# Optimization experiments

Measured on AMD Instinct MI355X. Metric: run time of the kernel, lower is better.

The kernel has to match this reference:

```python
import jax, jax.numpy as jnp
import numpy as np

D_MODEL = 1024
NUM_HEADS = 16
WINDOW = 2048  # must equal seq_len (see notes): source matmul attn(B,H,S,W) @ v(B,H,S,hd) requires W == S
SEQ_LEN = 2048
BATCH = 1


def setup_inputs() -> dict:
    key = jax.random.key(0)
    k0, k1, k2 = jax.random.split(key, 3)
    d = D_MODEL
    x = jax.random.normal(k0, (BATCH, SEQ_LEN, d), dtype=jnp.float32)
    w_qkv = jax.random.normal(k1, (3 * d, d), dtype=jnp.float32) * (d ** -0.5)
    b_qkv = jnp.zeros((3 * d,), dtype=jnp.float32)
    w_proj = jax.random.normal(k2, (d, d), dtype=jnp.float32) * (d ** -0.5)
    b_proj = jnp.zeros((d,), dtype=jnp.float32)
    return {"x": x, "w_qkv": w_qkv, "b_qkv": b_qkv, "w_proj": w_proj, "b_proj": b_proj}


def reference(x, w_qkv, b_qkv, w_proj, b_proj):
    B, S, d = x.shape
    H = NUM_HEADS
    hd = d // H
    W = WINDOW
    scale = hd ** -0.5

    # qkv projection (torch Linear: x @ W^T + b)
    qkv = x @ w_qkv.T + b_qkv                      # (B, S, 3d)
    qkv = qkv.reshape(B, S, 3, H, hd).transpose(2, 0, 3, 1, 4)  # (3, B, H, S, hd)
    q, k, v = qkv[0], qkv[1], qkv[2]

    # sliding-window scores: score[b,h,i,j] = q_i . k_padded[i+j] * scale, j in [0, W)
    pad = W // 2
    k_pad = jnp.pad(k, ((0, 0), (0, 0), (pad, pad), (0, 0)))     # (B, H, S+W, hd)
    scores_full = jnp.einsum('bhid,bhjd->bhij', q, k_pad) * scale  # (B, H, S, S+W)
    idx = jnp.arange(S)[:, None] + jnp.arange(W)[None, :]          # (S, W) banded gather indices
    scores = jnp.take_along_axis(scores_full, idx[None, None], axis=-1)  # (B, H, S, W)

    attn = jax.nn.softmax(scores, axis=-1)
    attn = jnp.nan_to_num(attn)  # faithful to torch.nan_to_num(attn, 0.0)

    # Faithful to the source: forward() does matmul(attn, v), i.e. column j of the
    # windowed attn indexes v position j directly (requires W == S).
    out = jnp.einsum('bhij,bhjd->bhid', attn, v)   # (B, H, S, hd)
    out = out.transpose(0, 2, 1, 3).reshape(B, S, d)
    out = out @ w_proj.T + b_proj
    return out, attn
```

## Files before the change

### kernel.cpp

```cpp
#include <hip/hip_runtime.h>
#include <hip/hip_bf16.h>

typedef __hip_bfloat16 bf16;
typedef __attribute__((ext_vector_type(8))) short short8;
typedef __attribute__((ext_vector_type(4))) float f32x4;

#define DEV static __device__ __forceinline__

static constexpr int SEQ = 2048;
static constexpr int DM  = 1024;
static constexpr int NH  = 16;
static constexpr int HD  = 64;
static constexpr int WIN = 2048;
static constexpr int PAD = 1024;

DEV void async16(const void* g, void* l) {
  __builtin_amdgcn_global_load_lds(
      (__attribute__((address_space(1))) void*)(g),
      (__attribute__((address_space(3))) void*)(l), 16, 0, 0);
}

__global__ __launch_bounds__(256) void k_cvt(const float* __restrict__ x,
                                             const float* __restrict__ wq,
                                             const float* __restrict__ wp,
                                             bf16* __restrict__ xb,
                                             bf16* __restrict__ wqb,
                                             bf16* __restrict__ wpb) {
  const int NX = SEQ * DM, NQ = 3 * DM * DM, NP = DM * DM;
  const int tot = (NX + NQ + NP) >> 2;
  const int stride = gridDim.x * 256;
  for (int i = blockIdx.x * 256 + threadIdx.x; i < tot; i += stride) {
    int e = i << 2;
    const float* s; bf16* d; int o;
    if (e < NX)            { s = x;  d = xb;  o = e; }
    else if (e < NX + NQ)  { s = wq; d = wqb; o = e - NX; }
    else                   { s = wp; d = wpb; o = e - NX - NQ; }
    float4 v = *(const float4*)(s + o);
    __align__(8) bf16 t4[4] = {__float2bfloat16(v.x), __float2bfloat16(v.y),
                               __float2bfloat16(v.z), __float2bfloat16(v.w)};
    *(uint2*)(d + o) = *(uint2*)t4;
  }
}

DEV void gemm_core(const bf16* __restrict__ A, const bf16* __restrict__ B,
                   int m0, int n0, int K, int tid, bf16* As, bf16* Bs,
                   f32x4 (&acc)[4][4]) {
  const int lane = tid & 63, wid = tid >> 6;
  const int wm = wid >> 1, wn = wid & 1;
  const int l15 = lane & 15, l4 = lane >> 4;
  for (int k0 = 0; k0 < K; k0 += 64) {
    __syncthreads();
    #pragma unroll
    for (int it = 0; it < 4; ++it) {
      int rb = it * 32 + wid * 8;
      int r  = rb + (lane >> 3);
      int c  = (lane & 7) * 8;
      async16(A + (size_t)(m0 + r) * K + k0 + c, As + rb * 64);
      async16(B + (size_t)(n0 + r) * K + k0 + c, Bs + rb * 64);
    }
    asm volatile("s_waitcnt vmcnt(0)" ::: "memory");
    __syncthreads();
    #pragma unroll
    for (int kk = 0; kk < 2; ++kk) {
      short8 a[4], b[4];
      #pragma unroll
      for (int im = 0; im < 4; ++im)
        a[im] = *(const short8*)(As + (wm * 64 + im * 16 + l15) * 64 + kk * 32 + l4 * 8);
      #pragma unroll
      for (int in = 0; in < 4; ++in)
        b[in] = *(const short8*)(Bs + (wn * 64 + in * 16 + l15) * 64 + kk * 32 + l4 * 8);
      #pragma unroll
      for (int im = 0; im < 4; ++im)
        #pragma unroll
        for (int in = 0; in < 4; ++in)
          acc[im][in] = __builtin_amdgcn_mfma_f32_16x16x32_bf16(a[im], b[in], acc[im][in], 0, 0, 0);
    }
  }
}

__global__ __launch_bounds__(256) void k_gemm_qkv(const bf16* __restrict__ A,
                                                  const bf16* __restrict__ B,
                                                  const float* __restrict__ bias,
                                                  bf16* __restrict__ qo,
                                                  bf16* __restrict__ ko,
                                                  bf16* __restrict__ vt) {
  __shared__ bf16 As[128 * 64], Bs[128 * 64];
  const int tid = threadIdx.x, lane = tid & 63;
  const int wid = tid >> 6, wm = wid >> 1, wn = wid & 1;
  const int l15 = lane & 15, l4 = lane >> 4;
  const int m0 = blockIdx.x * 128, n0 = blockIdx.y * 128;
  f32x4 acc[4][4] = {};
  gemm_core(A, B, m0, n0, DM, tid, As, Bs, acc);
  #pragma unroll
  for (int im = 0; im < 4; ++im)
    #pragma unroll
    for (int in = 0; in < 4; ++in) {
      int col = n0 + wn * 64 + in * 16 + l15;
      float bval = bias[col];
      int t = col >> 10, h = (col >> 6) & 15, dd = col & 63;
      int row0 = m0 + wm * 64 + im * 16 + l4 * 4;
      if (t == 2) {
        __align__(8) bf16 t4[4];
        #pragma unroll
        for (int r = 0; r < 4; ++r)
          t4[r] = __float2bfloat16(acc[im][in][r] + bval);
        *(uint2*)&vt[((size_t)h * HD + dd) * SEQ + row0] = *(uint2*)t4;
      } else {
        #pragma unroll
        for (int r = 0; r < 4; ++r) {
          float v = acc[im][in][r] + bval;
          size_t idx = ((size_t)h * SEQ + row0 + r) * HD + dd;
          if (t == 0) qo[idx] = __float2bfloat16(v * 0.18033688011112042f);
          else        ko[idx] = __float2bfloat16(v);
        }
      }
    }
}

DEV void stage_kp(const bf16* kbase, int i0, int tt, int lane, bf16* dst) {
  #pragma unroll
  for (int it = 0; it < 4; ++it) {
    int r  = it * 8 + (lane >> 3);
    int cg = lane & 7;
    int jp = i0 + tt * 32 + r;
    int krow = jp - PAD;
    krow = krow < 0 ? 0 : (krow > SEQ - 1 ? SEQ - 1 : krow);
    int sc = (cg ^ (r & 7)) * 8;
    async16(kbase + (size_t)krow * HD + sc, dst + it * 8 * 64);
  }
}

DEV void load_kf(const bf16* kbase, int i0, int tt, int l15, int l4,
                 short8 (&kf)[2][2]) {
  #pragma unroll
  for (int fn = 0; fn < 2; ++fn) {
    int jp = i0 + tt * 32 + fn * 16 + l15;
    int krow = jp - PAD;
    krow = krow < 0 ? 0 : (krow > SEQ - 1 ? SEQ - 1 : krow);
    const bf16* rp = kbase + (size_t)krow * HD + l4 * 8;
    kf[fn][0] = *(const short8*)(rp);
    kf[fn][1] = *(const short8*)(rp + 32);
  }
}

DEV void qk_mfma_sw(const short8 (&kf)[2][2], const short8 (&qf)[2][2],
                    f32x4 (&sf)[2][2]) {
  __builtin_amdgcn_s_setprio(1);
  #pragma unroll
  for (int kg = 0; kg < 2; ++kg)
    #pragma unroll
    for (int fj = 0; fj < 2; ++fj)
      #pragma unroll
      for (int fi = 0; fi < 2; ++fi)
        sf[fj][fi] = __builtin_amdgcn_mfma_f32_16x16x32_bf16(kf[fj][kg], qf[fi][kg], sf[fj][fi], 0, 0, 0);
  __builtin_amdgcn_s_setprio(0);
}

DEV int pad_lo(int i0) { int d = PAD - i0; return d <= 0 ? 0 : (d >> 5); }
DEV int pad_hi(int i0) { int t = ((PAD + SEQ - 1 - i0) >> 5) + 1; return t > 65 ? 65 : t; }

__global__ __launch_bounds__(64) void k_attn1(const bf16* __restrict__ q,
                                              const bf16* __restrict__ kkk,
                                              float* __restrict__ psums,
                                              float* __restrict__ aof) {
  const int c  = blockIdx.x & 3;
  const int i0 = ((blockIdx.x >> 2) & 63) << 5;
  const int h  = blockIdx.x >> 8;
  const int lane = threadIdx.x;
  const int l15 = lane & 15, l4 = lane >> 4;

  {
    f32x4 z = {0.f, 0.f, 0.f, 0.f};
    ((f32x4*)aof)[blockIdx.x * 128 + lane]      = z;
    ((f32x4*)aof)[blockIdx.x * 128 + 64 + lane] = z;
  }

  constexpr int st[5] = {0, 16, 32, 48, 65};
  const int lo_g = pad_lo(i0), hi_g = pad_hi(i0);
  int lo = st[c] > lo_g ? st[c] : lo_g;
  int hi = st[c + 1] < hi_g ? st[c + 1] : hi_g;

  short8 qf[2][2];
  #pragma unroll
  for (int fi = 0; fi < 2; ++fi)
    #pragma unroll
    for (int kg = 0; kg < 2; ++kg)
      qf[fi][kg] = *(const short8*)&q[((size_t)h * SEQ + i0 + fi * 16 + l15) * HD + kg * 32 + l4 * 8];

  const bf16* kbase = kkk + (size_t)h * SEQ * HD;

  float psum[2] = {0.f, 0.f};
  auto acc_tile = [&](const f32x4 (&sf)[2][2], int tt) {
    const bool interior = (tt >= 1) && (tt <= 63) &&
                          (i0 + tt * 32 >= PAD) && (i0 + tt * 32 + 31 < PAD + SEQ);
    if (interior) {
      #pragma unroll
      for (int fj = 0; fj < 2; ++fj)
        #pragma unroll
        for (int r = 0; r < 4; ++r) {
          psum[0] += __builtin_amdgcn_exp2f(sf[fj][0][r]);
          psum[1] += __builtin_amdgcn_exp2f(sf[fj][1][r]);
        }
    } else {
      #pragma unroll
      for (int fj = 0; fj < 2; ++fj)
        #pragma unroll
        for (int r = 0; r < 4; ++r) {
          int jj = tt * 32 + fj * 16 + l4 * 4 + r;
          int jp = i0 + jj;
          bool pad = (jp < PAD) || (jp >= PAD + SEQ);
          #pragma unroll
          for (int fi = 0; fi < 2; ++fi) {
            int iloc = fi * 16 + l15;
            float e = pad ? 1.0f : __builtin_amdgcn_exp2f(sf[fj][fi][r]);
            if ((unsigned)(jj - iloc) < (unsigned)WIN) psum[fi] += e;
          }
        }
    }
  };

  short8 kA[2][2], kB[2][2];
  if (lo < hi) load_kf(kbase, i0, lo, l15, l4, kA);
  for (int tt = lo; tt < hi; ++tt) {
    if (((tt - lo) & 1) == 0) {
      if (tt + 1 < hi) load_kf(kbase, i0, tt + 1, l15, l4, kB);
      f32x4 sf[2][2] = {};
      qk_mfma_sw(kA, qf, sf);
      acc_tile(sf, tt);
    } else {
      if (tt + 1 < hi) load_kf(kbase, i0, tt + 1, l15, l4, kA);
      f32x4 sf[2][2] = {};
      qk_mfma_sw(kB, qf, sf);
      acc_tile(sf, tt);
    }
  }

  float r0 = psum[0];
  r0 += __shfl_xor(r0, 16); r0 += __shfl_xor(r0, 32);
  float r1 = psum[1];
  r1 += __shfl_xor(r1, 16); r1 += __shfl_xor(r1, 32);
  if (lane < 32) {
    int i_abs = i0 + lane;
    float s = (lane < 16) ? r0 : r1;
    if (c == 0) {
      int cl = i0 + lo_g * 32 - i_abs; if (cl < 0) cl = 0;
      int cr = i_abs + WIN - (i0 + hi_g * 32); if (cr < 0) cr = 0;
      s += (float)(cl + cr);
    }
    psums[((size_t)c * NH + h) * SEQ + i_abs] = s;
  }
}

__global__ __launch_bounds__(64) void k_attn2(const bf16* __restrict__ q,
                                              const bf16* __restrict__ kkk,
                                              const bf16* __restrict__ vT,
                                              const float* __restrict__ psums,
                                              float* __restrict__ attn,
                                              float* __restrict__ aof) {
  const int c  = blockIdx.x & 3;
  const int i0 = ((blockIdx.x >> 2) & 63) << 5;
  const int h  = blockIdx.x >> 8;
  const int lane = threadIdx.x;
  const int l15 = lane & 15, l4 = lane >> 4;
  const int c0 = c * 16, c1 = c0 + 16;
  const int lo_g = pad_lo(i0), hi_g = pad_hi(i0);

  __shared__ bf16 KP[2][32 * 64];
  __shared__ float JF[32 * 64];

  float inv[2][4];
  #pragma unroll
  for (int fm = 0; fm < 2; ++fm)
    #pragma unroll
    for (int r = 0; r < 4; ++r) {
      int row = i0 + fm * 16 + l4 * 4 + r;
      float s = 0.f;
      #pragma unroll
      for (int cc = 0; cc < 4; ++cc)
        s += psums[((size_t)cc * NH + h) * SEQ + row];
      inv[fm][r] = __builtin_amdgcn_rcpf(s);
    }

  short8 qf[2][2];
  #pragma unroll
  for (int fm = 0; fm < 2; ++fm)
    #pragma unroll
    for (int kg = 0; kg < 2; ++kg)
      qf[fm][kg] = *(const short8*)&q[((size_t)h * SEQ + i0 + fm * 16 + l15) * HD + kg * 32 + l4 * 8];

  const bf16* kbase = kkk + (size_t)h * SEQ * HD;
  const bf16* vbase = vT + (size_t)h * HD * SEQ;
  float* abase = attn + (size_t)(h * SEQ + i0) * WIN;

  f32x4 oacc[2][4] = {};
  stage_kp(kbase, i0, c0, lane, KP[0]);
  for (int tt = c0; tt <= c1; ++tt) {
    short8 bv[4];
    if (tt > c0) {
      int jb = (tt - 1) * 32;
      #pragma unroll
      for (int nd = 0; nd < 4; ++nd)
        bv[nd] = *(const short8*)&vbase[(size_t)(nd * 16 + l15) * SEQ + jb + l4 * 8];
    }
    int nxt = (tt < c1) ? tt + 1 : tt;
    stage_kp(kbase, i0, nxt, lane, KP[(tt + 1) & 1]);
    if (tt == c0)          asm volatile("s_waitcnt vmcnt(4)" ::: "memory");
    else if (tt == c0 + 1) asm volatile("s_waitcnt vmcnt(8)" ::: "memory");
    else                   asm volatile("s_waitcnt vmcnt(12)" ::: "memory");

    const bool fp = (tt < lo_g) || (tt >= hi_g);
    f32x4 sf[2][2] = {};
    if (!fp) {
      const bf16* KPb = KP[tt & 1];
      __builtin_amdgcn_s_setprio(1);
      #pragma unroll
      for (int kg = 0; kg < 2; ++kg) {
        short8 kfr[2];
        #pragma unroll
        for (int fn = 0; fn < 2; ++fn) {
          int jl = fn * 16 + l15;
          int pg = (kg * 4 + l4) ^ (jl & 7);
          kfr[fn] = *(const short8*)&KPb[jl * 64 + pg * 8];
        }
        #pragma unroll
        for (int fm = 0; fm < 2; ++fm)
          #pragma unroll
          for (int fn = 0; fn < 2; ++fn)
            sf[fm][fn] = __builtin_amdgcn_mfma_f32_16x16x32_bf16(qf[fm][kg], kfr[fn], sf[fm][fn], 0, 0, 0);
      }
      __builtin_amdgcn_s_setprio(0);
    }

    const bool allv = (i0 + tt * 32 >= PAD) && (i0 + tt * 32 + 31 < PAD + SEQ);
    #pragma unroll
    for (int fm = 0; fm < 2; ++fm)
      #pragma unroll
      for (int fn = 0; fn < 2; ++fn) {
        int J0 = tt * 32 + fn * 16 + l15;
        bool padc = fp || (!allv && ((i0 + J0 < PAD) || (i0 + J0 >= PAD + SEQ)));
        #pragma unroll
        for (int r = 0; r < 4; ++r) {
          int row = fm * 16 + l4 * 4 + r;
          float e = padc ? 1.0f : __builtin_amdgcn_exp2f(sf[fm][fn][r]);
          float val = e * inv[fm][r];
          int j6 = (J0 - row) & 63;
          int pgrp = (j6 >> 2) ^ ((row & 7) << 1);
          JF[row * 64 + pgrp * 4 + (j6 & 3)] = val;
        }
      }

    if (tt > c0) {
      const int g = (tt - 1) & 1;
      const int Jb = (tt - 1) * 32;
      #pragma unroll
      for (int s = 0; s < 4; ++s) {
        int row = s * 8 + (lane >> 3);
        int c8 = lane & 7;
        int pgrp = (g * 8 + c8) ^ ((row & 7) << 1);
        f32x4 vv = *(const f32x4*)&JF[row * 64 + pgrp * 4];
        __builtin_nontemporal_store(vv, (f32x4*)(abase + (size_t)row * WIN + Jb + c8 * 4));
      }
      short8 af[2];
      #pragma unroll
      for (int fm = 0; fm < 2; ++fm) {
        int row = fm * 16 + l15;
        int pg0 = (g * 8 + l4 * 2) ^ ((row & 7) << 1);
        const float* p = &JF[row * 64 + pg0 * 4];
        union { unsigned short u[8]; short8 v; } tmp;
        #pragma unroll
        for (int e = 0; e < 8; ++e)
          tmp.u[e] = __bfloat16_as_ushort(__float2bfloat16(p[e]));
        af[fm] = tmp.v;
      }
      __builtin_amdgcn_s_setprio(1);
      #pragma unroll
      for (int fm = 0; fm < 2; ++fm)
        #pragma unroll
        for (int nd = 0; nd < 4; ++nd)
          oacc[fm][nd] = __builtin_amdgcn_mfma_f32_16x16x32_bf16(af[fm], bv[nd], oacc[fm][nd], 0, 0, 0);
      __builtin_amdgcn_s_setprio(0);
    }
  }
  #pragma unroll
  for (int fm = 0; fm < 2; ++fm)
    #pragma unroll
    for (int nd = 0; nd < 4; ++nd)
      #pragma unroll
      for (int r = 0; r < 4; ++r) {
        int i  = i0 + fm * 16 + l4 * 4 + r;
        int dd = nd * 16 + l15;
        atomicAdd(&aof[((size_t)h * SEQ + i) * HD + dd], oacc[fm][nd][r]);
      }
}

__global__ __launch_bounds__(256) void k_ored(const float* __restrict__ aof,
                                              bf16* __restrict__ ao) {
  int f = blockIdx.x * 256 + threadIdx.x;
  int e = f << 2;
  int h  = e >> 17;
  int i  = (e >> 6) & (SEQ - 1);
  int dd = e & 63;
  float4 v = ((const float4*)aof)[f];
  __align__(8) bf16 t4[4] = {__float2bfloat16(v.x), __float2bfloat16(v.y),
                             __float2bfloat16(v.z), __float2bfloat16(v.w)};
  *(uint2*)&ao[(size_t)i * DM + h * HD + dd] = *(uint2*)t4;
}

__global__ __launch_bounds__(256) void k_gemm_proj(const bf16* __restrict__ A,
                                                   const bf16* __restrict__ B,
                                                   const float* __restrict__ bias,
                                                   float* __restrict__ out) {
  __shared__ bf16 As[128 * 64], Bs[128 * 64];
  const int tid = threadIdx.x, lane = tid & 63;
  const int wid = tid >> 6, wm = wid >> 1, wn = wid & 1;
  const int l15 = lane & 15, l4 = lane >> 4;
  const int m0 = blockIdx.x * 128, n0 = blockIdx.y * 128;
  f32x4 acc[4][4] = {};
  gemm_core(A, B, m0, n0, DM, tid, As, Bs, acc);
  #pragma unroll
  for (int im = 0; im < 4; ++im)
    #pragma unroll
    for (int in = 0; in < 4; ++in) {
      int col = n0 + wn * 64 + in * 16 + l15;
      float bval = bias[col];
      #pragma unroll
      for (int r = 0; r < 4; ++r) {
        int row = m0 + wm * 64 + im * 16 + l4 * 4 + r;
        out[(size_t)row * DM + col] = acc[im][in][r] + bval;
      }
    }
}

extern "C" void kernel_launch(void* const* d_in, const int* in_sizes, int n_in,
                              void* d_out, int out_size, void* d_ws, size_t ws_size,
                              hipStream_t stream) {
  (void)in_sizes; (void)n_in; (void)out_size; (void)ws_size;
  const float* x  = (const float*)d_in[0];
  const float* wq = (const float*)d_in[1];
  const float* bq = (const float*)d_in[2];
  const float* wp = (const float*)d_in[3];
  const float* bp = (const float*)d_in[4];
  float* out  = (float*)d_out;
  float* attn = out + (size_t)SEQ * DM;

  char* ws = (char*)d_ws;
  bf16* xb    = (bf16*)(ws + (size_t) 0);
  bf16* wqb   = (bf16*)(ws + ((size_t)4  << 20));
  bf16* wpb   = (bf16*)(ws + ((size_t)10 << 20));
  bf16* qarr  = (bf16*)(ws + ((size_t)12 << 20));
  bf16* karr  = (bf16*)(ws + ((size_t)16 << 20));
  bf16* vt    = (bf16*)(ws + ((size_t)24 << 20));
  bf16* ao    = (bf16*)(ws + ((size_t)28 << 20));
  float* aof  = (float*)(ws + (size_t)0);
  float* psums= (float*)(ws + ((size_t)8 << 20));

  k_cvt<<<dim3(1024), dim3(256), 0, stream>>>(x, wq, wp, xb, wqb, wpb);
  k_gemm_qkv<<<dim3(16, 24), dim3(256), 0, stream>>>(xb, wqb, bq, qarr, karr, vt);
  k_attn1<<<dim3(4096), dim3(64), 0, stream>>>(qarr, karr, psums, aof);
  k_attn2<<<dim3(4096), dim3(64), 0, stream>>>(qarr, karr, vt, psums, attn, aof);
  k_ored<<<dim3(NH * SEQ * HD / 4 / 256), dim3(256), 0, stream>>>(aof, ao);
  k_gemm_proj<<<dim3(16, 8), dim3(256), 0, stream>>>(ao, wpb, bp, out);
}
```

Before: 176.8 us.

## Merge four chunk waves per attention block and stage K through LDS in pass one

Both attention kernels now launch 256-thread blocks in which each of four waves handles one column chunk of the same 32-row query tile, replacing four separate 64-thread blocks. Each wave gets its own LDS slices for K and JF. The first pass no longer loads K fragments directly from global into registers; it double-buffers K tiles into swizzled LDS with async global-to-LDS loads and a vmcnt wait, like the second pass already does. The goal is fewer, larger workgroups and cheaper K loads, at the cost of more LDS per block, which may limit occupancy.

```diff
diff --git a/kernel.cpp b/kernel.cpp
--- a/kernel.cpp
+++ b/kernel.cpp
@@ -130,49 +130,69 @@
   }
 }
 
-DEV void load_kf(const bf16* kbase, int i0, int tt, int l15, int l4,
-                 short8 (&kf)[2][2]) {
-  #pragma unroll
-  for (int fn = 0; fn < 2; ++fn) {
-    int jp = i0 + tt * 32 + fn * 16 + l15;
-    int krow = jp - PAD;
-    krow = krow < 0 ? 0 : (krow > SEQ - 1 ? SEQ - 1 : krow);
-    const bf16* rp = kbase + (size_t)krow * HD + l4 * 8;
-    kf[fn][0] = *(const short8*)(rp);
-    kf[fn][1] = *(const short8*)(rp + 32);
-  }
-}
-
-DEV void qk_mfma_sw(const short8 (&kf)[2][2], const short8 (&qf)[2][2],
-                    f32x4 (&sf)[2][2]) {
+DEV void qk_mfma_lds(const bf16* KPb, const short8 (&qf)[2][2], int l15, int l4,
+                     f32x4 (&sf)[2][2]) {
   __builtin_amdgcn_s_setprio(1);
   #pragma unroll
-  for (int kg = 0; kg < 2; ++kg)
+  for (int kg = 0; kg < 2; ++kg) {
+    short8 kfr[2];
+    #pragma unroll
+    for (int fn = 0; fn < 2; ++fn) {
+      int jl = fn * 16 + l15;
+      int pg = (kg * 4 + l4) ^ (jl & 7);
+      kfr[fn] = *(const short8*)&KPb[jl * 64 + pg * 8];
+    }
+    #pragma unroll
+    for (int fm = 0; fm < 2; ++fm)
+      #pragma unroll
+      for (int fn = 0; fn < 2; ++fn)
+        sf[fm][fn] = __builtin_amdgcn_mfma_f32_16x16x32_bf16(qf[fm][kg], kfr[fn], sf[fm][fn], 0, 0, 0);
+  }
+  __builtin_amdgcn_s_setprio(0);
+}
+
+DEV void qk_mfma_lds_sw(const bf16* KPb, const short8 (&qf)[2][2], int l15, int l4,
+                        f32x4 (&sf)[2][2]) {
+  __builtin_amdgcn_s_setprio(1);
+  #pragma unroll
+  for (int kg = 0; kg < 2; ++kg) {
+    short8 kfr[2];
+    #pragma unroll
+    for (int fj = 0; fj < 2; ++fj) {
+      int jl = fj * 16 + l15;
+      int pg = (kg * 4 + l4) ^ (jl & 7);
+      kfr[fj] = *(const short8*)&KPb[jl * 64 + pg * 8];
+    }
     #pragma unroll
     for (int fj = 0; fj < 2; ++fj)
       #pragma unroll
       for (int fi = 0; fi < 2; ++fi)
-        sf[fj][fi] = __builtin_amdgcn_mfma_f32_16x16x32_bf16(kf[fj][kg], qf[fi][kg], sf[fj][fi], 0, 0, 0);
+        sf[fj][fi] = __builtin_amdgcn_mfma_f32_16x16x32_bf16(kfr[fj], qf[fi][kg], sf[fj][fi], 0, 0, 0);
+  }
   __builtin_amdgcn_s_setprio(0);
 }
 
 DEV int pad_lo(int i0) { int d = PAD - i0; return d <= 0 ? 0 : (d >> 5); }
 DEV int pad_hi(int i0) { int t = ((PAD + SEQ - 1 - i0) >> 5) + 1; return t > 65 ? 65 : t; }
 
-__global__ __launch_bounds__(64) void k_attn1(const bf16* __restrict__ q,
-                                              const bf16* __restrict__ kkk,
-                                              float* __restrict__ psums,
-                                              float* __restrict__ aof) {
-  const int c  = blockIdx.x & 3;
-  const int i0 = ((blockIdx.x >> 2) & 63) << 5;
-  const int h  = blockIdx.x >> 8;
-  const int lane = threadIdx.x;
+__global__ __launch_bounds__(256) void k_attn1(const bf16* __restrict__ q,
+                                               const bf16* __restrict__ kkk,
+                                               float* __restrict__ psums,
+                                               float* __restrict__ aof) {
+  const int h  = blockIdx.x >> 6;
+  const int i0 = (blockIdx.x & 63) << 5;
+  const int tid = threadIdx.x;
+  const int c = tid >> 6;
+  const int lane = tid & 63;
   const int l15 = lane & 15, l4 = lane >> 4;
+
+  __shared__ bf16 KP[4][2][32 * 64];
 
   {
     f32x4 z = {0.f, 0.f, 0.f, 0.f};
-    ((f32x4*)aof)[blockIdx.x * 128 + lane]      = z;
-    ((f32x4*)aof)[blockIdx.x * 128 + 64 + lane] = z;
+    size_t zb = ((size_t)h * SEQ + i0) * (HD / 4);
+    ((f32x4*)aof)[zb + tid]       = z;
+    ((f32x4*)aof)[zb + 256 + tid] = z;
   }
 
   constexpr int st[5] = {0, 16, 32, 48, 65};
@@ -190,51 +210,42 @@
   const bf16* kbase = kkk + (size_t)h * SEQ * HD;
 
   float psum[2] = {0.f, 0.f};
-  auto acc_tile = [&](const f32x4 (&sf)[2][2], int tt) {
-    const bool interior = (tt >= 1) && (tt <= 63) &&
-                          (i0 + tt * 32 >= PAD) && (i0 + tt * 32 + 31 < PAD + SEQ);
-    if (interior) {
-      #pragma unroll
-      for (int fj = 0; fj < 2; ++fj)
-        #pragma unroll
-        for (int r = 0; r < 4; ++r) {
-          psum[0] += __builtin_amdgcn_exp2f(sf[fj][0][r]);
-          psum[1] += __builtin_amdgcn_exp2f(sf[fj][1][r]);
-        }
-    } else {
-      #pragma unroll
-      for (int fj = 0; fj < 2; ++fj)
-        #pragma unroll
-        for (int r = 0; r < 4; ++r) {
-          int jj = tt * 32 + fj * 16 + l4 * 4 + r;
-          int jp = i0 + jj;
-          bool pad = (jp < PAD) || (jp >= PAD + SEQ);
+  if (lo < hi) {
+    stage_kp(kbase, i0, lo, lane, KP[c][lo & 1]);
+    for (int tt = lo; tt < hi; ++tt) {
+      int nxt = (tt + 1 < hi) ? tt + 1 : tt;
+      stage_kp(kbase, i0, nxt, lane, KP[c][(tt + 1) & 1]);
+      asm volatile("s_waitcnt vmcnt(4)" ::: "memory");
+      f32x4 sf[2][2] = {};
+      qk_mfma_lds_sw(KP[c][tt & 1], qf, l15, l4, sf);
+      const bool interior = (tt >= 1) && (tt <= 63) &&
+                            (i0 + tt * 32 >= PAD) && (i0 + tt * 32 + 31 < PAD + SEQ);
+      if (interior) {
+        #pragma unroll
+        for (int fj = 0; fj < 2; ++fj)
           #pragma unroll
-          for (int fi = 0; fi < 2; ++fi) {
-            int iloc = fi * 16 + l15;
-            float e = pad ? 1.0f : __builtin_amdgcn_exp2f(sf[fj][fi][r]);
-            if ((unsigned)(jj - iloc) < (unsigned)WIN) psum[fi] += e;
+          for (int r = 0; r < 4; ++r) {
+            psum[0] += __builtin_amdgcn_exp2f(sf[fj][0][r]);
+            psum[1] += __builtin_amdgcn_exp2f(sf[fj][1][r]);
           }
-        }
-    }
-  };
-
-  short8 kA[2][2], kB[2][2];
-  if (lo < hi) load_kf(kbase, i0, lo, l15, l4, kA);
-  for (int tt = lo; tt < hi; ++tt) {
-    if (((tt - lo) & 1) == 0) {
-      if (tt + 1 < hi) load_kf(kbase, i0, tt + 1, l15, l4, kB);
-      f32x4 sf[2][2] = {};
-      qk_mfma_sw(kA, qf, sf);
-      acc_tile(sf, tt);
-    } else {
-      if (tt + 1 < hi) load_kf(kbase, i0, tt + 1, l15, l4, kA);
-      f32x4 sf[2][2] = {};
-      qk_mfma_sw(kB, qf, sf);
-      acc_tile(sf, tt);
-    }
-  }
-
+      } else {
+        #pragma unroll
+        for (int fj = 0; fj < 2; ++fj)
+          #pragma unroll
+          for (int r = 0; r < 4; ++r) {
+            int jj = tt * 32 + fj * 16 + l4 * 4 + r;
+            int jp = i0 + jj;
+            bool pad = (jp < PAD) || (jp >= PAD + SEQ);
+            #pragma unroll
+            for (int fi = 0; fi < 2; ++fi) {
+              int iloc = fi * 16 + l15;
+              float e = pad ? 1.0f : __builtin_amdgcn_exp2f(sf[fj][fi][r]);
+              if ((unsigned)(jj - iloc) < (unsigned)WIN) psum[fi] += e;
+            }
+          }
+      }
+    }
+  }
   float r0 = psum[0];
   r0 += __shfl_xor(r0, 16); r0 += __shfl_xor(r0, 32);
   float r1 = psum[1];
@@ -251,22 +262,23 @@
   }
 }
 
-__global__ __launch_bounds__(64) void k_attn2(const bf16* __restrict__ q,
-                                              const bf16* __restrict__ kkk,
-                                              const bf16* __restrict__ vT,
-                                              const float* __restrict__ psums,
-                                              float* __restrict__ attn,
-                                              float* __restrict__ aof) {
-  const int c  = blockIdx.x & 3;
-  const int i0 = ((blockIdx.x >> 2) & 63) << 5;
-  const int h  = blockIdx.x >> 8;
-  const int lane = threadIdx.x;
+__global__ __launch_bounds__(256) void k_attn2(const bf16* __restrict__ q,
+                                               const bf16* __restrict__ kkk,
+                                               const bf16* __restrict__ vT,
+                                               const float* __restrict__ psums,
+                                               float* __restrict__ attn,
+                                               float* __restrict__ aof) {
+  const int h  = blockIdx.x >> 6;
+  const int i0 = (blockIdx.x & 63) << 5;
+  const int tid = threadIdx.x;
+  const int c = tid >> 6;
+  const int lane = tid & 63;
   const int l15 = lane & 15, l4 = lane >> 4;
   const int c0 = c * 16, c1 = c0 + 16;
   const int lo_g = pad_lo(i0), hi_g = pad_hi(i0);
 
-  __shared__ bf16 KP[2][32 * 64];
-  __shared__ float JF[32 * 64];
+  __shared__ bf16 KP[4][2][32 * 64];
+  __shared__ float JF[4][32 * 64];
 
   float inv[2][4];
   #pragma unroll
@@ -291,9 +303,10 @@
   const bf16* kbase = kkk + (size_t)h * SEQ * HD;
   const bf16* vbase = vT + (size_t)h * HD * SEQ;
   float* abase = attn + (size_t)(h * SEQ + i0) * WIN;
+  float* JFW = JF[c];
 
   f32x4 oacc[2][4] = {};
-  stage_kp(kbase, i0, c0, lane, KP[0]);
+  stage_kp(kbase, i0, c0, lane, KP[c][0]);
   for (int tt = c0; tt <= c1; ++tt) {
     short8 bv[4];
     if (tt > c0) {
@@ -303,33 +316,14 @@
         bv[nd] = *(const short8*)&vbase[(size_t)(nd * 16 + l15) * SEQ + jb + l4 * 8];
     }
     int nxt = (tt < c1) ? tt + 1 : tt;
-    stage_kp(kbase, i0, nxt, lane, KP[(tt + 1) & 1]);
+    stage_kp(kbase, i0, nxt, lane, KP[c][(tt + 1) & 1]);
     if (tt == c0)          asm volatile("s_waitcnt vmcnt(4)" ::: "memory");
     else if (tt == c0 + 1) asm volatile("s_waitcnt vmcnt(8)" ::: "memory");
     else                   asm volatile("s_waitcnt vmcnt(12)" ::: "memory");
 
     const bool fp = (tt < lo_g) || (tt >= hi_g);
     f32x4 sf[2][2] = {};
-    if (!fp) {
-      const bf16* KPb = KP[tt & 1];
-      __builtin_amdgcn_s_setprio(1);
-      #pragma unroll
-      for (int kg = 0; kg < 2; ++kg) {
-        short8 kfr[2];
-        #pragma unroll
-        for (int fn = 0; fn < 2; ++fn) {
-          int jl = fn * 16 + l15;
-          int pg = (kg * 4 + l4) ^ (jl & 7);
-          kfr[fn] = *(const short8*)&KPb[jl * 64 + pg * 8];
-        }
-        #pragma unroll
-        for (int fm = 0; fm < 2; ++fm)
-          #pragma unroll
-          for (int fn = 0; fn < 2; ++fn)
-            sf[fm][fn] = __builtin_amdgcn_mfma_f32_16x16x32_bf16(qf[fm][kg], kfr[fn], sf[fm][fn], 0, 0, 0);
-      }
-      __builtin_amdgcn_s_setprio(0);
-    }
+    if (!fp) qk_mfma_lds(KP[c][tt & 1], qf, l15, l4, sf);
 
     const bool allv = (i0 + tt * 32 >= PAD) && (i0 + tt * 32 + 31 < PAD + SEQ);
     #pragma unroll
@@ -345,7 +339,7 @@
           float val = e * inv[fm][r];
           int j6 = (J0 - row) & 63;
           int pgrp = (j6 >> 2) ^ ((row & 7) << 1);
-          JF[row * 64 + pgrp * 4 + (j6 & 3)] = val;
+          JFW[row * 64 + pgrp * 4 + (j6 & 3)] = val;
         }
       }
 
@@ -357,7 +351,7 @@
         int row = s * 8 + (lane >> 3);
         int c8 = lane & 7;
         int pgrp = (g * 8 + c8) ^ ((row & 7) << 1);
-        f32x4 vv = *(const f32x4*)&JF[row * 64 + pgrp * 4];
+        f32x4 vv = *(const f32x4*)&JFW[row * 64 + pgrp * 4];
         __builtin_nontemporal_store(vv, (f32x4*)(abase + (size_t)row * WIN + Jb + c8 * 4));
       }
       short8 af[2];
@@ -365,7 +359,7 @@
       for (int fm = 0; fm < 2; ++fm) {
         int row = fm * 16 + l15;
         int pg0 = (g * 8 + l4 * 2) ^ ((row & 7) << 1);
-        const float* p = &JF[row * 64 + pg0 * 4];
+        const float* p = &JFW[row * 64 + pg0 * 4];
         union { unsigned short u[8]; short8 v; } tmp;
         #pragma unroll
         for (int e = 0; e < 8; ++e)
@@ -456,8 +450,8 @@
 
   k_cvt<<<dim3(1024), dim3(256), 0, stream>>>(x, wq, wp, xb, wqb, wpb);
   k_gemm_qkv<<<dim3(16, 24), dim3(256), 0, stream>>>(xb, wqb, bq, qarr, karr, vt);
-  k_attn1<<<dim3(4096), dim3(64), 0, stream>>>(qarr, karr, psums, aof);
-  k_attn2<<<dim3(4096), dim3(64), 0, stream>>>(qarr, karr, vt, psums, attn, aof);
+  k_attn1<<<dim3(1024), dim3(256), 0, stream>>>(qarr, karr, psums, aof);
+  k_attn2<<<dim3(1024), dim3(256), 0, stream>>>(qarr, karr, vt, psums, attn, aof);
   k_ored<<<dim3(NH * SEQ * HD / 4 / 256), dim3(256), 0, stream>>>(aof, ao);
   k_gemm_proj<<<dim3(16, 8), dim3(256), 0, stream>>>(ao, wpb, bp, out);
 }
```

New measurement: 162.6 us. -8.0%, faster.
